# Optimization experiments

Measured on AMD Instinct MI355X. Metric: run time of the kernel, lower is better.

## Reference

```python
import jax, jax.numpy as jnp
import numpy as np

V, BLOCK, L, H, E = 1000, 1024, 8, 16, 1024
D = E // H
HID = 4 * E
B, S = 4, 1024
NEG = -1e9


def setup_inputs() -> dict:
    key = jax.random.key(0)
    ks = jax.random.split(key, 10)
    s = 0.02
    rn = lambda k, shp: jax.random.normal(k, shp, jnp.float32) * s
    return dict(
        idx=jax.random.randint(ks[0], (B, S), 0, V),
        wte=rn(ks[1], (V, E)),
        wpe=rn(ks[2], (BLOCK, E)),
        ln1_w=jnp.ones((L, E), jnp.float32), ln1_b=jnp.zeros((L, E), jnp.float32),
        qkv_w=rn(ks[3], (L, E, 3 * E)), qkv_b=jnp.zeros((L, 3 * E), jnp.float32),
        out_w=rn(ks[4], (L, E, E)), out_b=jnp.zeros((L, E), jnp.float32),
        ln2_w=jnp.ones((L, E), jnp.float32), ln2_b=jnp.zeros((L, E), jnp.float32),
        fc1_w=rn(ks[5], (L, E, HID)), fc1_b=jnp.zeros((L, HID), jnp.float32),
        fc2_w=rn(ks[6], (L, HID, E)), fc2_b=jnp.zeros((L, E), jnp.float32),
        lnf_w=jnp.ones((E,), jnp.float32), lnf_b=jnp.zeros((E,), jnp.float32),
        head_w=rn(ks[7], (E, V)), head_b=jnp.zeros((V,), jnp.float32),
    )


def _ln(x, w, b):
    m = x.mean(-1, keepdims=True)
    v = x.var(-1, keepdims=True)
    return (x - m) / jnp.sqrt(v + 1e-5) * w + b


def _block(x, p):
    (ln1_w, ln1_b, qkv_w, qkv_b, out_w, out_b,
     ln2_w, ln2_b, fc1_w, fc1_b, fc2_w, fc2_b) = p
    b, s, _ = x.shape
    # --- causal self-attention ---
    h = _ln(x, ln1_w, ln1_b)
    qkv = h @ qkv_w + qkv_b                           # [b, s, 3E]
    q, k, v = jnp.split(qkv, 3, axis=-1)
    q = q.reshape(b, s, H, D)
    k = k.reshape(b, s, H, D)
    v = v.reshape(b, s, H, D)
    att = jnp.einsum('bqhd,bkhd->bhqk', q, k) / np.sqrt(D).astype(np.float32)
    mask = jnp.tril(jnp.ones((s, s), bool))
    att = jnp.where(mask, att, NEG)
    att = jax.nn.softmax(att, axis=-1)
    y = jnp.einsum('bhqk,bkhd->bqhd', att, v).reshape(b, s, E)
    x = x + (y @ out_w + out_b)
    # --- MLP ---
    h = _ln(x, ln2_w, ln2_b)
    h = jax.nn.gelu(h @ fc1_w + fc1_b, approximate=False)
    x = x + (h @ fc2_w + fc2_b)
    return x


def reference(idx, wte, wpe, ln1_w, ln1_b, qkv_w, qkv_b, out_w, out_b,
              ln2_w, ln2_b, fc1_w, fc1_b, fc2_w, fc2_b, lnf_w, lnf_b,
              head_w, head_b):
    s = idx.shape[1]
    x = wte[idx] + wpe[:s]                            # [B, S, E]
    layer_params = (ln1_w, ln1_b, qkv_w, qkv_b, out_w, out_b,
                    ln2_w, ln2_b, fc1_w, fc1_b, fc2_w, fc2_b)
    def step(x, p):
        return _block(x, p), None
    x, _ = jax.lax.scan(step, x, layer_params)
    x = _ln(x, lnf_w, lnf_b)
    logits = x @ head_w + head_b                      # [B, S, V]
    return logits
```

## Files before the change

kernel.cpp:

```cpp
#include <hip/hip_runtime.h>
#include <math.h>


typedef unsigned short u16;
typedef unsigned int u32;
typedef __attribute__((ext_vector_type(4))) float f32x4;
typedef __attribute__((ext_vector_type(8))) __bf16 bf16x8;
typedef __attribute__((ext_vector_type(8))) u16 u16x8;
typedef __attribute__((ext_vector_type(4))) u16 u16x4;

#define E 1024
#define HID 4096
#define NH 16
#define HD 64
#define SEQ 1024
#define NB 4
#define NL 8
#define MTOK 4096
#define VOC 1000

#define VMCNT(n) asm volatile("s_waitcnt vmcnt(" #n ")" ::: "memory")

__device__ __forceinline__ u16 f2bf(float f){
  u32 u = __float_as_uint(f);
  u32 r = (u + 0x7fffu + ((u >> 16) & 1u)) >> 16;
  return (u16)r;
}
__device__ __forceinline__ float bf2f(u16 b){
  return __uint_as_float((u32)b << 16);
}
__device__ __forceinline__ bf16x8 ld_bf8(const u16* p){
  return *reinterpret_cast<const bf16x8*>(p);
}
__device__ __forceinline__ bf16x8 as_bf(u16x8 v){
  return __builtin_bit_cast(bf16x8, v);
}

__device__ __forceinline__ void gload16(const void* g, void* l){
  __builtin_amdgcn_global_load_lds(
      (const __attribute__((address_space(1))) void*)g,
      (__attribute__((address_space(3))) void*)l, 16, 0, 0);
}

__global__ __launch_bounds__(256) void embed_kernel(
    const int* __restrict__ idx, const float* __restrict__ wte,
    const float* __restrict__ wpe, float* __restrict__ x)
{
  int tok = blockIdx.x, tid = threadIdx.x;
  int id = idx[tok];
  int s = tok & (SEQ - 1);
  f32x4 a = *reinterpret_cast<const f32x4*>(&wte[(size_t)id * E + tid * 4]);
  f32x4 p = *reinterpret_cast<const f32x4*>(&wpe[(size_t)s * E + tid * 4]);
  f32x4 r = a + p;
  *reinterpret_cast<f32x4*>(&x[(size_t)tok * E + tid * 4]) = r;
}

__global__ __launch_bounds__(256) void ln_kernel(
    const float* __restrict__ x, const float* __restrict__ w,
    const float* __restrict__ b, u16* __restrict__ h)
{
  int row = blockIdx.x, tid = threadIdx.x;
  const float* xr = x + (size_t)row * E;
  f32x4 v = *reinterpret_cast<const f32x4*>(xr + tid * 4);
  float s = v[0] + v[1] + v[2] + v[3];
  float q = v[0]*v[0] + v[1]*v[1] + v[2]*v[2] + v[3]*v[3];
  #pragma unroll
  for (int mm = 1; mm < 64; mm <<= 1){
    s += __shfl_xor(s, mm);
    q += __shfl_xor(q, mm);
  }
  __shared__ float red[8];
  int wv = tid >> 6;
  if ((tid & 63) == 0){ red[wv] = s; red[4 + wv] = q; }
  __syncthreads();
  s = red[0] + red[1] + red[2] + red[3];
  q = red[4] + red[5] + red[6] + red[7];
  float mean = s * (1.0f / E);
  float var = q * (1.0f / E) - mean * mean;
  float rstd = rsqrtf(var + 1e-5f);
  f32x4 wv4 = *reinterpret_cast<const f32x4*>(w + tid * 4);
  f32x4 bv4 = *reinterpret_cast<const f32x4*>(b + tid * 4);
  u16 o0 = f2bf((v[0] - mean) * rstd * wv4[0] + bv4[0]);
  u16 o1 = f2bf((v[1] - mean) * rstd * wv4[1] + bv4[1]);
  u16 o2 = f2bf((v[2] - mean) * rstd * wv4[2] + bv4[2]);
  u16 o3 = f2bf((v[3] - mean) * rstd * wv4[3] + bv4[3]);
  u16* hp = &h[(size_t)row * E + tid * 4];
  hp[0] = o0; hp[1] = o1; hp[2] = o2; hp[3] = o3;
}

__global__ __launch_bounds__(256) void wconv_kernel(
    const float* __restrict__ W, u16* __restrict__ Wt,
    int K, int Nsrc, int N)
{
  __shared__ float T[64][65];
  const int tid = threadIdx.x;
  const int n0 = blockIdx.x * 64, k0 = blockIdx.y * 64;
  const int c = (tid & 15) * 4, rbase = tid >> 4;
  if (n0 + 64 <= Nsrc){
    #pragma unroll
    for (int p = 0; p < 4; p++){
      int r = rbase + p * 16;
      f32x4 v = *reinterpret_cast<const f32x4*>(&W[(size_t)(k0 + r) * Nsrc + n0 + c]);
      T[r][c] = v[0]; T[r][c+1] = v[1]; T[r][c+2] = v[2]; T[r][c+3] = v[3];
    }
  } else {
    #pragma unroll
    for (int p = 0; p < 4; p++){
      int r = rbase + p * 16;
      #pragma unroll
      for (int j = 0; j < 4; j++){
        int n = n0 + c + j;
        T[r][c + j] = (n < Nsrc) ? W[(size_t)(k0 + r) * Nsrc + n] : 0.0f;
      }
    }
  }
  __syncthreads();
  const int nr = tid >> 2, ks = (tid & 3) * 16;
  u16x8 o0, o1;
  #pragma unroll
  for (int i = 0; i < 8; i++){
    o0[i] = f2bf(T[ks + i][nr]);
    o1[i] = f2bf(T[ks + 8 + i][nr]);
  }
  u16* dst = &Wt[(size_t)(n0 + nr) * K + k0 + ks];
  *reinterpret_cast<u16x8*>(dst) = o0;
  *reinterpret_cast<u16x8*>(dst + 8) = o1;
}

enum { EPI_BF16 = 0, EPI_GELU = 1, EPI_RESID = 2, EPI_OUT = 3 };

template<int EPI, int NW, int NWX, int FM, int FN, int MINW>
__global__ __launch_bounds__(NW * 64, MINW) void gemm2_kernel(
    const u16* __restrict__ A, const u16* __restrict__ Wt,
    const float* __restrict__ bias, void* __restrict__ outp,
    float* __restrict__ xres, int M, int N, int K)
{
  constexpr int BM = FM * 16 * (NW / NWX);
  constexpr int BN = FN * 16 * NWX;
  constexpr int SLOT = (BM + BN) * 32;
  constexpr int RPW = (BM + BN) / 16 / NW;
  extern __shared__ u16 lds[];

  const int tid = threadIdx.x;
  const int lane = tid & 63, w = tid >> 6;
  const int l15 = lane & 15, g = lane >> 4;
  const int wr = w / NWX, wc = w % NWX;
  const int wrbase = wr * FM * 16, wcbase = wc * FN * 16;

  const int nwgx = gridDim.x;
  const int bid = blockIdx.y * nwgx + blockIdx.x;
  const int cpx = (nwgx * gridDim.y) >> 3;
  const int swz = (bid & 7) * cpx + (bid >> 3);
  const int bm = (swz / nwgx) * BM, bn = (swz % nwgx) * BN;

  const u16* Abase = A + (size_t)bm * K;
  const u16* Bbase = Wt + (size_t)bn * K;

  f32x4 acc[FM][FN];
  #pragma unroll
  for (int i = 0; i < FM; i++)
    #pragma unroll
    for (int j = 0; j < FN; j++)
      acc[i][j] = f32x4{0.f, 0.f, 0.f, 0.f};

  const int lr = lane >> 2, ps = lane & 3;
  const int ss = ps ^ ((lane >> 4) & 3);
  auto STAGE = [&](int s, int cc){
    const int k0 = cc * 32;
    u16* As = lds + s * SLOT;
    u16* Bs = As + BM * 32;
    #pragma unroll
    for (int j = 0; j < RPW; j++){
      int base = (w * RPW + j) * 16;
      if (base < BM){
        gload16(&Abase[(size_t)(base + lr) * K + k0 + ss * 8], As + base * 32);
      } else {
        int rb = base - BM;
        gload16(&Bbase[(size_t)(rb + lr) * K + k0 + ss * 8], Bs + rb * 32);
      }
    }
  };

  const int nt = K >> 5;
  STAGE(0, 0);
  STAGE(1, 1);
  int sl = 0;
  for (int c = 0; c < nt; c++){
    if (c + 1 < nt){
      if constexpr (RPW == 3) { VMCNT(3); } else { VMCNT(4); }
    } else {
      VMCNT(0);
    }
    __builtin_amdgcn_sched_barrier(0);
    __builtin_amdgcn_s_barrier();
    __builtin_amdgcn_sched_barrier(0);

    const u16* As = lds + sl * SLOT;
    const u16* Bs = As + BM * 32;
    bf16x8 af[FM], bf[FN];
    const int rsw = (g ^ (l15 >> 2)) * 8;
    #pragma unroll
    for (int mf = 0; mf < FM; mf++)
      af[mf] = ld_bf8(&As[(wrbase + mf * 16 + l15) * 32 + rsw]);
    #pragma unroll
    for (int nf = 0; nf < FN; nf++)
      bf[nf] = ld_bf8(&Bs[(wcbase + nf * 16 + l15) * 32 + rsw]);
    __builtin_amdgcn_s_setprio(1);
    #pragma unroll
    for (int mf = 0; mf < FM; mf++)
      #pragma unroll
      for (int nf = 0; nf < FN; nf++)
        acc[mf][nf] = __builtin_amdgcn_mfma_f32_16x16x32_bf16(
            af[mf], bf[nf], acc[mf][nf], 0, 0, 0);
    __builtin_amdgcn_s_setprio(0);

    if (c + 2 < nt){
      int s2 = sl + 2; if (s2 >= 3) s2 -= 3;
      STAGE(s2, c + 2);
    }
    sl++; if (sl >= 3) sl -= 3;
  }

  #pragma unroll
  for (int mf = 0; mf < FM; mf++){
    #pragma unroll
    for (int nf = 0; nf < FN; nf++){
      int col = bn + wcbase + nf * 16 + l15;
      float bv = bias[col];
      #pragma unroll
      for (int r = 0; r < 4; r++){
        int row = bm + wrbase + mf * 16 + g * 4 + r;
        float v = acc[mf][nf][r] + bv;
        if constexpr (EPI == EPI_BF16){
          ((u16*)outp)[(size_t)row * N + col] = f2bf(v);
        } else if constexpr (EPI == EPI_GELU){
          ((u16*)outp)[(size_t)row * N + col] =
              f2bf(0.5f * v * (1.0f + erff(v * 0.70710678118654752f)));
        } else if constexpr (EPI == EPI_RESID){
          xres[(size_t)row * N + col] += v;
        } else {
          if (col < VOC)
            ((float*)outp)[(size_t)row * VOC + col] = v;
        }
      }
    }
  }
}

__global__ __launch_bounds__(256) void attn_kernel(
    const u16* __restrict__ qkv, u16* __restrict__ y)
{
  __shared__ u16 Kl[64 * 64];
  __shared__ u16 Vt[64 * 72];
  __shared__ u16 Pl[4 * 16 * 72];
  const int pr = blockIdx.x, hh = blockIdx.y, b = blockIdx.z;
  const int tid = threadIdx.x;
  const int lane = tid & 63, w = tid >> 6;
  const int l15 = lane & 15, g = lane >> 4;
  const size_t tokbase = (size_t)b * SEQ;
  const int qstart[2] = { pr * 64, (15 - pr) * 64 };

  int qbase[2], dt[2];
  u16x8 q0[2], q1[2];
  f32x4 o[2][4];
  float m[2][4], llp[2][4];
  #pragma unroll
  for (int st = 0; st < 2; st++){
    qbase[st] = qstart[st] + w * 16;
    dt[st] = qbase[st] >> 6;
    const u16* qp = &qkv[(tokbase + qbase[st] + l15) * (3 * E) + hh * HD];
    u16x8 ra = *reinterpret_cast<const u16x8*>(&qp[g * 8]);
    u16x8 rb = *reinterpret_cast<const u16x8*>(&qp[32 + g * 8]);
    #pragma unroll
    for (int j = 0; j < 8; j++){
      q0[st][j] = f2bf(bf2f(ra[j]) * 0.125f);
      q1[st][j] = f2bf(bf2f(rb[j]) * 0.125f);
    }
    #pragma unroll
    for (int dc = 0; dc < 4; dc++) o[st][dc] = f32x4{0.f, 0.f, 0.f, 0.f};
    #pragma unroll
    for (int r = 0; r < 4; r++){ m[st][r] = -1e30f; llp[st][r] = 0.f; }
  }

  u16* Pw = &Pl[w * 16 * 72];
  const int T = 16 - pr;

  for (int t = 0; t < T; t++){
    const int k0 = t * 64;
    __syncthreads();
    #pragma unroll
    for (int j = 0; j < 2; j++){
      int row = w * 16 + j * 8 + (lane >> 3);
      int sl = lane & 7;
      const u16* src = &qkv[(tokbase + k0 + row) * (3 * E) + E + hh * HD
                            + ((sl ^ (row & 7)) * 8)];
      gload16(src, &Kl[w * 1024 + j * 512]);
    }
    {
      int d0 = (tid & 15) * 4;
      int s  = tid >> 4;
      #pragma unroll
      for (int mh = 0; mh < 2; mh++){
        int kA = s + 32 * mh;
        const u16* vpA = &qkv[(tokbase + k0 + kA) * (3 * E) + 2 * E + hh * HD + d0];
        const u16* vpB = vpA + 16 * (3 * E);
        u16x4 va = *reinterpret_cast<const u16x4*>(vpA);
        u16x4 vb = *reinterpret_cast<const u16x4*>(vpB);
        #pragma unroll
        for (int i = 0; i < 4; i++)
          *reinterpret_cast<u32*>(&Vt[(d0 + i) * 72 + 4 * s + 2 * mh]) =
              (u32)va[i] | ((u32)vb[i] << 16);
      }
    }
    __syncthreads();

    #pragma unroll
    for (int st = 0; st < 2; st++){
      if (t > dt[st]) continue;
      const bool diag = (t == dt[st]);
      f32x4 s[4];
      #pragma unroll
      for (int kg = 0; kg < 4; kg++){
        int key = kg * 16 + l15;
        const u16* kb = &Kl[key * 64];
        bf16x8 k0f = ld_bf8(&kb[(g ^ (key & 7)) * 8]);
        bf16x8 k1f = ld_bf8(&kb[((4 + g) ^ (key & 7)) * 8]);
        f32x4 z = f32x4{0.f, 0.f, 0.f, 0.f};
        z = __builtin_amdgcn_mfma_f32_16x16x32_bf16(as_bf(q0[st]), k0f, z, 0, 0, 0);
        z = __builtin_amdgcn_mfma_f32_16x16x32_bf16(as_bf(q1[st]), k1f, z, 0, 0, 0);
        s[kg] = z;
      }
      if (diag){
        #pragma unroll
        for (int kg = 0; kg < 4; kg++){
          int key = k0 + kg * 16 + l15;
          #pragma unroll
          for (int r = 0; r < 4; r++){
            int q = qbase[st] + g * 4 + r;
            s[kg][r] = (key <= q) ? s[kg][r] : -1e9f;
          }
        }
      }
      float lmax[4];
      bool need = false;
      #pragma unroll
      for (int r = 0; r < 4; r++){
        lmax[r] = fmaxf(fmaxf(s[0][r], s[1][r]), fmaxf(s[2][r], s[3][r]));
        need = need || (lmax[r] > m[st][r] + 8.0f);
      }
      if (__any(need)){
        #pragma unroll
        for (int r = 0; r < 4; r++){
          float x = lmax[r];
          x = fmaxf(x, __shfl_xor(x, 1));
          x = fmaxf(x, __shfl_xor(x, 2));
          x = fmaxf(x, __shfl_xor(x, 4));
          x = fmaxf(x, __shfl_xor(x, 8));
          float mn = fmaxf(m[st][r], x);
          float al = __expf(m[st][r] - mn);
          m[st][r] = mn;
          llp[st][r] *= al;
          #pragma unroll
          for (int dc = 0; dc < 4; dc++) o[st][dc][r] *= al;
        }
      }
      #pragma unroll
      for (int r = 0; r < 4; r++){
        float p0 = __expf(s[0][r] - m[st][r]);
        float p1 = __expf(s[1][r] - m[st][r]);
        float p2 = __expf(s[2][r] - m[st][r]);
        float p3 = __expf(s[3][r] - m[st][r]);
        llp[st][r] += (p0 + p1) + (p2 + p3);
        u16x4 pp = { f2bf(p0), f2bf(p1), f2bf(p2), f2bf(p3) };
        *reinterpret_cast<u16x4*>(&Pw[(g * 4 + r) * 72 + 4 * l15]) = pp;
      }
      bf16x8 pa0 = ld_bf8(&Pw[l15 * 72 + g * 8]);
      bf16x8 pa1 = ld_bf8(&Pw[l15 * 72 + 32 + g * 8]);
      #pragma unroll
      for (int dc = 0; dc < 4; dc++){
        bf16x8 v0 = ld_bf8(&Vt[(dc * 16 + l15) * 72 + g * 8]);
        bf16x8 v1 = ld_bf8(&Vt[(dc * 16 + l15) * 72 + 32 + g * 8]);
        o[st][dc] = __builtin_amdgcn_mfma_f32_16x16x32_bf16(pa0, v0, o[st][dc], 0, 0, 0);
        o[st][dc] = __builtin_amdgcn_mfma_f32_16x16x32_bf16(pa1, v1, o[st][dc], 0, 0, 0);
      }
    }
  }

  #pragma unroll
  for (int st = 0; st < 2; st++){
    #pragma unroll
    for (int r = 0; r < 4; r++){
      float rs = llp[st][r];
      rs += __shfl_xor(rs, 1);
      rs += __shfl_xor(rs, 2);
      rs += __shfl_xor(rs, 4);
      rs += __shfl_xor(rs, 8);
      float inv = 1.0f / rs;
      int row = qbase[st] + g * 4 + r;
      #pragma unroll
      for (int dc = 0; dc < 4; dc++){
        int col = hh * HD + dc * 16 + l15;
        y[(tokbase + row) * E + col] = f2bf(o[st][dc][r] * inv);
      }
    }
  }
}

__global__ __launch_bounds__(256) void biaspad_kernel(
    const float* __restrict__ hb, float* __restrict__ bpad)
{
  int i = blockIdx.x * 256 + threadIdx.x;
  if (i < 1024) bpad[i] = (i < VOC) ? hb[i] : 0.0f;
}

extern "C" void kernel_launch(void* const* d_in, const int* in_sizes, int n_in,
                              void* d_out, int out_size, void* d_ws, size_t ws_size,
                              hipStream_t stream)
{
  const int*   idx    = (const int*)  d_in[0];
  const float* wte    = (const float*)d_in[1];
  const float* wpe    = (const float*)d_in[2];
  const float* ln1_w  = (const float*)d_in[3];
  const float* ln1_b  = (const float*)d_in[4];
  const float* qkv_w  = (const float*)d_in[5];
  const float* qkv_b  = (const float*)d_in[6];
  const float* out_w  = (const float*)d_in[7];
  const float* out_b  = (const float*)d_in[8];
  const float* ln2_w  = (const float*)d_in[9];
  const float* ln2_b  = (const float*)d_in[10];
  const float* fc1_w  = (const float*)d_in[11];
  const float* fc1_b  = (const float*)d_in[12];
  const float* fc2_w  = (const float*)d_in[13];
  const float* fc2_b  = (const float*)d_in[14];
  const float* lnf_w  = (const float*)d_in[15];
  const float* lnf_b  = (const float*)d_in[16];
  const float* head_w = (const float*)d_in[17];
  const float* head_b = (const float*)d_in[18];

  char* ws = (char*)d_ws;
  float* x    = (float*)(ws + 0);
  u16*   h    = (u16*)  (ws + 16777216);
  u16*   qkvb = (u16*)  (ws + 25165824);
  u16*   y    = (u16*)  (ws + 50331648);
  u16*   g    = (u16*)  (ws + 58720256);
  u16*   wq   = (u16*)  (ws + 92274688);
  u16*   wo   = (u16*)  (ws + 98566144);
  u16*   w1   = (u16*)  (ws + 100663296);
  u16*   w2   = (u16*)  (ws + 109051904);
  u16*   wh   = (u16*)  (ws + 117440512);
  float* hbp  = (float*)(ws + 119537664);

  constexpr int LDS_BIG = 3 * (384 * 32) * 2;
  constexpr int LDS_SML = 3 * (256 * 32) * 2;
  hipFuncSetAttribute((const void*)gemm2_kernel<EPI_BF16, 8, 4, 4, 4, 4>,
                      hipFuncAttributeMaxDynamicSharedMemorySize, LDS_BIG);
  hipFuncSetAttribute((const void*)gemm2_kernel<EPI_GELU, 8, 4, 4, 4, 4>,
                      hipFuncAttributeMaxDynamicSharedMemorySize, LDS_BIG);

  embed_kernel<<<MTOK, 256, 0, stream>>>(idx, wte, wpe, x);
  biaspad_kernel<<<4, 256, 0, stream>>>(head_b, hbp);

  for (int l = 0; l < NL; l++){
    ln_kernel<<<MTOK, 256, 0, stream>>>(x, ln1_w + l * E, ln1_b + l * E, h);
    wconv_kernel<<<dim3(48, 16), 256, 0, stream>>>(
        qkv_w + (size_t)l * E * 3 * E, wq, E, 3 * E, 3 * E);
    gemm2_kernel<EPI_BF16, 8, 4, 4, 4, 4><<<dim3(12, 32), 512, LDS_BIG, stream>>>(
        h, wq, qkv_b + (size_t)l * 3 * E, qkvb, nullptr, MTOK, 3 * E, E);
    attn_kernel<<<dim3(8, NH, NB), 256, 0, stream>>>(qkvb, y);
    wconv_kernel<<<dim3(16, 16), 256, 0, stream>>>(
        out_w + (size_t)l * E * E, wo, E, E, E);
    gemm2_kernel<EPI_RESID, 4, 2, 4, 4, 3><<<dim3(8, 32), 256, LDS_SML, stream>>>(
        y, wo, out_b + (size_t)l * E, nullptr, x, MTOK, E, E);
    ln_kernel<<<MTOK, 256, 0, stream>>>(x, ln2_w + l * E, ln2_b + l * E, h);
    wconv_kernel<<<dim3(64, 16), 256, 0, stream>>>(
        fc1_w + (size_t)l * E * HID, w1, E, HID, HID);
    gemm2_kernel<EPI_GELU, 8, 4, 4, 4, 4><<<dim3(16, 32), 512, LDS_BIG, stream>>>(
        h, w1, fc1_b + (size_t)l * HID, g, nullptr, MTOK, HID, E);
    wconv_kernel<<<dim3(16, 64), 256, 0, stream>>>(
        fc2_w + (size_t)l * HID * E, w2, HID, E, E);
    gemm2_kernel<EPI_RESID, 4, 2, 4, 4, 3><<<dim3(8, 32), 256, LDS_SML, stream>>>(
        g, w2, fc2_b + (size_t)l * E, nullptr, x, MTOK, E, HID);
  }
  ln_kernel<<<MTOK, 256, 0, stream>>>(x, lnf_w, lnf_b, h);
  wconv_kernel<<<dim3(16, 16), 256, 0, stream>>>(head_w, wh, E, VOC, E);
  gemm2_kernel<EPI_OUT, 4, 2, 4, 4, 3><<<dim3(8, 32), 256, LDS_SML, stream>>>(
      h, wh, hbp, (float*)d_out, nullptr, MTOK, E, E);
}
```

Measured before the change: 2.003 ms.

## Unify GEMM to 128x128 tiles with five-stage LDS prefetch pipeline

```diff
diff --git a/kernel.cpp b/kernel.cpp
--- a/kernel.cpp
+++ b/kernel.cpp
@@ -129,23 +129,22 @@
 
 enum { EPI_BF16 = 0, EPI_GELU = 1, EPI_RESID = 2, EPI_OUT = 3 };
 
-template<int EPI, int NW, int NWX, int FM, int FN, int MINW>
-__global__ __launch_bounds__(NW * 64, MINW) void gemm2_kernel(
+template<int EPI>
+__global__ __launch_bounds__(256, 2) void gemm2_kernel(
     const u16* __restrict__ A, const u16* __restrict__ Wt,
     const float* __restrict__ bias, void* __restrict__ outp,
     float* __restrict__ xres, int M, int N, int K)
 {
-  constexpr int BM = FM * 16 * (NW / NWX);
-  constexpr int BN = FN * 16 * NWX;
+  constexpr int BM = 128, BN = 128;
   constexpr int SLOT = (BM + BN) * 32;
-  constexpr int RPW = (BM + BN) / 16 / NW;
+  constexpr int NS = 5;
+  constexpr int RPW = 4;
   extern __shared__ u16 lds[];
 
   const int tid = threadIdx.x;
   const int lane = tid & 63, w = tid >> 6;
   const int l15 = lane & 15, g = lane >> 4;
-  const int wr = w / NWX, wc = w % NWX;
-  const int wrbase = wr * FM * 16, wcbase = wc * FN * 16;
+  const int wrbase = (w >> 1) * 64, wcbase = (w & 1) * 64;
 
   const int nwgx = gridDim.x;
   const int bid = blockIdx.y * nwgx + blockIdx.x;
@@ -156,11 +155,11 @@
   const u16* Abase = A + (size_t)bm * K;
   const u16* Bbase = Wt + (size_t)bn * K;
 
-  f32x4 acc[FM][FN];
-  #pragma unroll
-  for (int i = 0; i < FM; i++)
-    #pragma unroll
-    for (int j = 0; j < FN; j++)
+  f32x4 acc[4][4];
+  #pragma unroll
+  for (int i = 0; i < 4; i++)
+    #pragma unroll
+    for (int j = 0; j < 4; j++)
       acc[i][j] = f32x4{0.f, 0.f, 0.f, 0.f};
 
   const int lr = lane >> 2, ps = lane & 3;
@@ -182,49 +181,48 @@
   };
 
   const int nt = K >> 5;
-  STAGE(0, 0);
-  STAGE(1, 1);
+  STAGE(0, 0); STAGE(1, 1); STAGE(2, 2); STAGE(3, 3);
   int sl = 0;
   for (int c = 0; c < nt; c++){
-    if (c + 1 < nt){
-      if constexpr (RPW == 3) { VMCNT(3); } else { VMCNT(4); }
-    } else {
-      VMCNT(0);
-    }
+    const int rem = nt - 1 - c;
+    if (rem >= 3)      { VMCNT(12); }
+    else if (rem == 2) { VMCNT(8); }
+    else if (rem == 1) { VMCNT(4); }
+    else               { VMCNT(0); }
     __builtin_amdgcn_sched_barrier(0);
     __builtin_amdgcn_s_barrier();
     __builtin_amdgcn_sched_barrier(0);
 
     const u16* As = lds + sl * SLOT;
     const u16* Bs = As + BM * 32;
-    bf16x8 af[FM], bf[FN];
+    bf16x8 af[4], bf[4];
     const int rsw = (g ^ (l15 >> 2)) * 8;
     #pragma unroll
-    for (int mf = 0; mf < FM; mf++)
+    for (int mf = 0; mf < 4; mf++)
       af[mf] = ld_bf8(&As[(wrbase + mf * 16 + l15) * 32 + rsw]);
     #pragma unroll
-    for (int nf = 0; nf < FN; nf++)
+    for (int nf = 0; nf < 4; nf++)
       bf[nf] = ld_bf8(&Bs[(wcbase + nf * 16 + l15) * 32 + rsw]);
     __builtin_amdgcn_s_setprio(1);
     #pragma unroll
-    for (int mf = 0; mf < FM; mf++)
-      #pragma unroll
-      for (int nf = 0; nf < FN; nf++)
+    for (int mf = 0; mf < 4; mf++)
+      #pragma unroll
+      for (int nf = 0; nf < 4; nf++)
         acc[mf][nf] = __builtin_amdgcn_mfma_f32_16x16x32_bf16(
             af[mf], bf[nf], acc[mf][nf], 0, 0, 0);
     __builtin_amdgcn_s_setprio(0);
 
-    if (c + 2 < nt){
-      int s2 = sl + 2; if (s2 >= 3) s2 -= 3;
-      STAGE(s2, c + 2);
-    }
-    sl++; if (sl >= 3) sl -= 3;
-  }
-
-  #pragma unroll
-  for (int mf = 0; mf < FM; mf++){
-    #pragma unroll
-    for (int nf = 0; nf < FN; nf++){
+    if (c + 4 < nt){
+      int s4 = sl + 4; if (s4 >= NS) s4 -= NS;
+      STAGE(s4, c + 4);
+    }
+    sl++; if (sl >= NS) sl -= NS;
+  }
+
+  #pragma unroll
+  for (int mf = 0; mf < 4; mf++){
+    #pragma unroll
+    for (int nf = 0; nf < 4; nf++){
       int col = bn + wcbase + nf * 16 + l15;
       float bv = bias[col];
       #pragma unroll
@@ -450,12 +448,15 @@
   u16*   wh   = (u16*)  (ws + 117440512);
   float* hbp  = (float*)(ws + 119537664);
 
-  constexpr int LDS_BIG = 3 * (384 * 32) * 2;
-  constexpr int LDS_SML = 3 * (256 * 32) * 2;
-  hipFuncSetAttribute((const void*)gemm2_kernel<EPI_BF16, 8, 4, 4, 4, 4>,
-                      hipFuncAttributeMaxDynamicSharedMemorySize, LDS_BIG);
-  hipFuncSetAttribute((const void*)gemm2_kernel<EPI_GELU, 8, 4, 4, 4, 4>,
-                      hipFuncAttributeMaxDynamicSharedMemorySize, LDS_BIG);
+  constexpr int LDS_UNI = 5 * (256 * 32) * 2;
+  hipFuncSetAttribute((const void*)gemm2_kernel<EPI_BF16>,
+                      hipFuncAttributeMaxDynamicSharedMemorySize, LDS_UNI);
+  hipFuncSetAttribute((const void*)gemm2_kernel<EPI_GELU>,
+                      hipFuncAttributeMaxDynamicSharedMemorySize, LDS_UNI);
+  hipFuncSetAttribute((const void*)gemm2_kernel<EPI_RESID>,
+                      hipFuncAttributeMaxDynamicSharedMemorySize, LDS_UNI);
+  hipFuncSetAttribute((const void*)gemm2_kernel<EPI_OUT>,
+                      hipFuncAttributeMaxDynamicSharedMemorySize, LDS_UNI);
 
   embed_kernel<<<MTOK, 256, 0, stream>>>(idx, wte, wpe, x);
   biaspad_kernel<<<4, 256, 0, stream>>>(head_b, hbp);
@@ -464,25 +465,25 @@
     ln_kernel<<<MTOK, 256, 0, stream>>>(x, ln1_w + l * E, ln1_b + l * E, h);
     wconv_kernel<<<dim3(48, 16), 256, 0, stream>>>(
         qkv_w + (size_t)l * E * 3 * E, wq, E, 3 * E, 3 * E);
-    gemm2_kernel<EPI_BF16, 8, 4, 4, 4, 4><<<dim3(12, 32), 512, LDS_BIG, stream>>>(
+    gemm2_kernel<EPI_BF16><<<dim3(24, 32), 256, LDS_UNI, stream>>>(
         h, wq, qkv_b + (size_t)l * 3 * E, qkvb, nullptr, MTOK, 3 * E, E);
     attn_kernel<<<dim3(8, NH, NB), 256, 0, stream>>>(qkvb, y);
     wconv_kernel<<<dim3(16, 16), 256, 0, stream>>>(
         out_w + (size_t)l * E * E, wo, E, E, E);
-    gemm2_kernel<EPI_RESID, 4, 2, 4, 4, 3><<<dim3(8, 32), 256, LDS_SML, stream>>>(
+    gemm2_kernel<EPI_RESID><<<dim3(8, 32), 256, LDS_UNI, stream>>>(
         y, wo, out_b + (size_t)l * E, nullptr, x, MTOK, E, E);
     ln_kernel<<<MTOK, 256, 0, stream>>>(x, ln2_w + l * E, ln2_b + l * E, h);
     wconv_kernel<<<dim3(64, 16), 256, 0, stream>>>(
         fc1_w + (size_t)l * E * HID, w1, E, HID, HID);
-    gemm2_kernel<EPI_GELU, 8, 4, 4, 4, 4><<<dim3(16, 32), 512, LDS_BIG, stream>>>(
+    gemm2_kernel<EPI_GELU><<<dim3(32, 32), 256, LDS_UNI, stream>>>(
         h, w1, fc1_b + (size_t)l * HID, g, nullptr, MTOK, HID, E);
     wconv_kernel<<<dim3(16, 64), 256, 0, stream>>>(
         fc2_w + (size_t)l * HID * E, w2, HID, E, E);
-    gemm2_kernel<EPI_RESID, 4, 2, 4, 4, 3><<<dim3(8, 32), 256, LDS_SML, stream>>>(
+    gemm2_kernel<EPI_RESID><<<dim3(8, 32), 256, LDS_UNI, stream>>>(
         g, w2, fc2_b + (size_t)l * E, nullptr, x, MTOK, E, HID);
   }
   ln_kernel<<<MTOK, 256, 0, stream>>>(x, lnf_w, lnf_b, h);
   wconv_kernel<<<dim3(16, 16), 256, 0, stream>>>(head_w, wh, E, VOC, E);
-  gemm2_kernel<EPI_OUT, 4, 2, 4, 4, 3><<<dim3(8, 32), 256, LDS_SML, stream>>>(
+  gemm2_kernel<EPI_OUT><<<dim3(8, 32), 256, LDS_UNI, stream>>>(
       h, wh, hbp, (float*)d_out, nullptr, MTOK, E, E);
 }
```

Measured after the change: 2.122 ms. 1.06x slower.

## Merge per-layer weight conversions; enlarge big GEMM tiles with four-stage pipeline

Applied to the files above, without the earlier changes.

```diff
diff --git a/kernel.cpp b/kernel.cpp
--- a/kernel.cpp
+++ b/kernel.cpp
@@ -88,6 +88,42 @@
   hp[0] = o0; hp[1] = o1; hp[2] = o2; hp[3] = o3;
 }
 
+__global__ __launch_bounds__(256) void wconv4_kernel(
+    const float* __restrict__ qw, const float* __restrict__ ow,
+    const float* __restrict__ f1, const float* __restrict__ f2,
+    u16* __restrict__ dq, u16* __restrict__ dо_unused, u16* __restrict__ d1,
+    u16* __restrict__ d2, u16* __restrict__ dw_out)
+{
+  const int bid = blockIdx.x, tid = threadIdx.x;
+  const float* W; u16* Wt; int K, Nsrc, nx, base;
+  if (bid < 768)      { W = qw; Wt = dq;     K = 1024; Nsrc = 3072; nx = 48; base = 0; }
+  else if (bid < 1024){ W = ow; Wt = dw_out; K = 1024; Nsrc = 1024; nx = 16; base = 768; }
+  else if (bid < 2048){ W = f1; Wt = d1;     K = 1024; Nsrc = 4096; nx = 64; base = 1024; }
+  else                { W = f2; Wt = d2;     K = 4096; Nsrc = 1024; nx = 16; base = 2048; }
+  const int t = bid - base;
+  const int n0 = (t % nx) * 64, k0 = (t / nx) * 64;
+
+  __shared__ float T[64][65];
+  const int c = (tid & 15) * 4, rbase = tid >> 4;
+  #pragma unroll
+  for (int p = 0; p < 4; p++){
+    int r = rbase + p * 16;
+    f32x4 v = *reinterpret_cast<const f32x4*>(&W[(size_t)(k0 + r) * Nsrc + n0 + c]);
+    T[r][c] = v[0]; T[r][c+1] = v[1]; T[r][c+2] = v[2]; T[r][c+3] = v[3];
+  }
+  __syncthreads();
+  const int nr = tid >> 2, ks = (tid & 3) * 16;
+  u16x8 o0, o1;
+  #pragma unroll
+  for (int i = 0; i < 8; i++){
+    o0[i] = f2bf(T[ks + i][nr]);
+    o1[i] = f2bf(T[ks + 8 + i][nr]);
+  }
+  u16* dst = &Wt[(size_t)(n0 + nr) * K + k0 + ks];
+  *reinterpret_cast<u16x8*>(dst) = o0;
+  *reinterpret_cast<u16x8*>(dst + 8) = o1;
+}
+
 __global__ __launch_bounds__(256) void wconv_kernel(
     const float* __restrict__ W, u16* __restrict__ Wt,
     int K, int Nsrc, int N)
@@ -96,22 +132,13 @@
   const int tid = threadIdx.x;
   const int n0 = blockIdx.x * 64, k0 = blockIdx.y * 64;
   const int c = (tid & 15) * 4, rbase = tid >> 4;
-  if (n0 + 64 <= Nsrc){
-    #pragma unroll
-    for (int p = 0; p < 4; p++){
-      int r = rbase + p * 16;
-      f32x4 v = *reinterpret_cast<const f32x4*>(&W[(size_t)(k0 + r) * Nsrc + n0 + c]);
-      T[r][c] = v[0]; T[r][c+1] = v[1]; T[r][c+2] = v[2]; T[r][c+3] = v[3];
-    }
-  } else {
-    #pragma unroll
-    for (int p = 0; p < 4; p++){
-      int r = rbase + p * 16;
-      #pragma unroll
-      for (int j = 0; j < 4; j++){
-        int n = n0 + c + j;
-        T[r][c + j] = (n < Nsrc) ? W[(size_t)(k0 + r) * Nsrc + n] : 0.0f;
-      }
+  #pragma unroll
+  for (int p = 0; p < 4; p++){
+    int r = rbase + p * 16;
+    #pragma unroll
+    for (int j = 0; j < 4; j++){
+      int n = n0 + c + j;
+      T[r][c + j] = (n < Nsrc) ? W[(size_t)(k0 + r) * Nsrc + n] : 0.0f;
     }
   }
   __syncthreads();
@@ -129,7 +156,7 @@
 
 enum { EPI_BF16 = 0, EPI_GELU = 1, EPI_RESID = 2, EPI_OUT = 3 };
 
-template<int EPI, int NW, int NWX, int FM, int FN, int MINW>
+template<int EPI, int NW, int NWX, int FM, int FN, int NS, int MINW>
 __global__ __launch_bounds__(NW * 64, MINW) void gemm2_kernel(
     const u16* __restrict__ A, const u16* __restrict__ Wt,
     const float* __restrict__ bias, void* __restrict__ outp,
@@ -184,12 +211,17 @@
   const int nt = K >> 5;
   STAGE(0, 0);
   STAGE(1, 1);
+  if constexpr (NS == 4) STAGE(2, 2);
   int sl = 0;
   for (int c = 0; c < nt; c++){
-    if (c + 1 < nt){
-      if constexpr (RPW == 3) { VMCNT(3); } else { VMCNT(4); }
+    const int rem = nt - 1 - c;
+    if constexpr (NS == 4){
+      if (rem >= 2)      { VMCNT(8); }
+      else if (rem == 1) { VMCNT(4); }
+      else               { VMCNT(0); }
     } else {
-      VMCNT(0);
+      if (rem >= 1)      { VMCNT(4); }
+      else               { VMCNT(0); }
     }
     __builtin_amdgcn_sched_barrier(0);
     __builtin_amdgcn_s_barrier();
@@ -214,11 +246,11 @@
             af[mf], bf[nf], acc[mf][nf], 0, 0, 0);
     __builtin_amdgcn_s_setprio(0);
 
-    if (c + 2 < nt){
-      int s2 = sl + 2; if (s2 >= 3) s2 -= 3;
-      STAGE(s2, c + 2);
-    }
-    sl++; if (sl >= 3) sl -= 3;
+    if (c + NS - 1 < nt){
+      int s2 = sl + NS - 1; if (s2 >= NS) s2 -= NS;
+      STAGE(s2, c + NS - 1);
+    }
+    sl++; if (sl >= NS) sl -= NS;
   }
 
   #pragma unroll
@@ -450,11 +482,11 @@
   u16*   wh   = (u16*)  (ws + 117440512);
   float* hbp  = (float*)(ws + 119537664);
 
-  constexpr int LDS_BIG = 3 * (384 * 32) * 2;
+  constexpr int LDS_BIG = 4 * (512 * 32) * 2;
   constexpr int LDS_SML = 3 * (256 * 32) * 2;
-  hipFuncSetAttribute((const void*)gemm2_kernel<EPI_BF16, 8, 4, 4, 4, 4>,
+  hipFuncSetAttribute((const void*)gemm2_kernel<EPI_BF16, 8, 4, 8, 4, 4, 2>,
                       hipFuncAttributeMaxDynamicSharedMemorySize, LDS_BIG);
-  hipFuncSetAttribute((const void*)gemm2_kernel<EPI_GELU, 8, 4, 4, 4, 4>,
+  hipFuncSetAttribute((const void*)gemm2_kernel<EPI_GELU, 8, 4, 8, 4, 4, 2>,
                       hipFuncAttributeMaxDynamicSharedMemorySize, LDS_BIG);
 
   embed_kernel<<<MTOK, 256, 0, stream>>>(idx, wte, wpe, x);
@@ -462,27 +494,23 @@
 
   for (int l = 0; l < NL; l++){
     ln_kernel<<<MTOK, 256, 0, stream>>>(x, ln1_w + l * E, ln1_b + l * E, h);
-    wconv_kernel<<<dim3(48, 16), 256, 0, stream>>>(
-        qkv_w + (size_t)l * E * 3 * E, wq, E, 3 * E, 3 * E);
-    gemm2_kernel<EPI_BF16, 8, 4, 4, 4, 4><<<dim3(12, 32), 512, LDS_BIG, stream>>>(
+    wconv4_kernel<<<3072, 256, 0, stream>>>(
+        qkv_w + (size_t)l * E * 3 * E, out_w + (size_t)l * E * E,
+        fc1_w + (size_t)l * E * HID, fc2_w + (size_t)l * HID * E,
+        wq, nullptr, w1, w2, wo);
+    gemm2_kernel<EPI_BF16, 8, 4, 8, 4, 4, 2><<<dim3(12, 16), 512, LDS_BIG, stream>>>(
         h, wq, qkv_b + (size_t)l * 3 * E, qkvb, nullptr, MTOK, 3 * E, E);
     attn_kernel<<<dim3(8, NH, NB), 256, 0, stream>>>(qkvb, y);
-    wconv_kernel<<<dim3(16, 16), 256, 0, stream>>>(
-        out_w + (size_t)l * E * E, wo, E, E, E);
-    gemm2_kernel<EPI_RESID, 4, 2, 4, 4, 3><<<dim3(8, 32), 256, LDS_SML, stream>>>(
+    gemm2_kernel<EPI_RESID, 4, 2, 4, 4, 3, 3><<<dim3(8, 32), 256, LDS_SML, stream>>>(
         y, wo, out_b + (size_t)l * E, nullptr, x, MTOK, E, E);
     ln_kernel<<<MTOK, 256, 0, stream>>>(x, ln2_w + l * E, ln2_b + l * E, h);
-    wconv_kernel<<<dim3(64, 16), 256, 0, stream>>>(
-        fc1_w + (size_t)l * E * HID, w1, E, HID, HID);
-    gemm2_kernel<EPI_GELU, 8, 4, 4, 4, 4><<<dim3(16, 32), 512, LDS_BIG, stream>>>(
+    gemm2_kernel<EPI_GELU, 8, 4, 8, 4, 4, 2><<<dim3(16, 16), 512, LDS_BIG, stream>>>(
         h, w1, fc1_b + (size_t)l * HID, g, nullptr, MTOK, HID, E);
-    wconv_kernel<<<dim3(16, 64), 256, 0, stream>>>(
-        fc2_w + (size_t)l * HID * E, w2, HID, E, E);
-    gemm2_kernel<EPI_RESID, 4, 2, 4, 4, 3><<<dim3(8, 32), 256, LDS_SML, stream>>>(
+    gemm2_kernel<EPI_RESID, 4, 2, 4, 4, 3, 3><<<dim3(8, 32), 256, LDS_SML, stream>>>(
         g, w2, fc2_b + (size_t)l * E, nullptr, x, MTOK, E, HID);
   }
   ln_kernel<<<MTOK, 256, 0, stream>>>(x, lnf_w, lnf_b, h);
   wconv_kernel<<<dim3(16, 16), 256, 0, stream>>>(head_w, wh, E, VOC, E);
-  gemm2_kernel<EPI_OUT, 4, 2, 4, 4, 3><<<dim3(8, 32), 256, LDS_SML, stream>>>(
+  gemm2_kernel<EPI_OUT, 4, 2, 4, 4, 3, 3><<<dim3(8, 32), 256, LDS_SML, stream>>>(
       h, wh, hbp, (float*)d_out, nullptr, MTOK, E, E);
 }
```

After: 1.977 ms. No clear change (-1.3%).
